# Optimization experiments

Hardware: AMD Instinct MI355X
Metric: run time of the kernel (lower is better)

## Reference

```python
import jax, jax.numpy as jnp
import numpy as np

N = 100000       # nodes
E = 1600000      # edges (before self-loops)
IN = 128         # input feature dim
HID = 16         # per-head hidden dim (layer 1)
HEADS = 8        # heads (layer 1)
OUT = 64         # output classes (layer 2, heads=1)
NEG_SLOPE = 0.2  # PyG GATConv default leaky relu slope


def setup_inputs() -> dict:
    key = jax.random.key(0)
    ks = jax.random.split(key, 10)
    s = 0.05
    return {
        "x": jax.random.normal(ks[0], (N, IN), jnp.float32),
        "edge_index": jax.random.randint(ks[1], (2, E), 0, N, dtype=jnp.int64),
        "W1": jax.random.normal(ks[2], (IN, HEADS * HID), jnp.float32) * s,
        "att_src1": jax.random.normal(ks[3], (HEADS, HID), jnp.float32) * s,
        "att_dst1": jax.random.normal(ks[4], (HEADS, HID), jnp.float32) * s,
        "bias1": jnp.zeros((HEADS * HID,), jnp.float32),
        "W2": jax.random.normal(ks[5], (HEADS * HID, OUT), jnp.float32) * s,
        "att_src2": jax.random.normal(ks[6], (1, OUT), jnp.float32) * s,
        "att_dst2": jax.random.normal(ks[7], (1, OUT), jnp.float32) * s,
        "bias2": jnp.zeros((OUT,), jnp.float32),
    }


def gat_conv(x, edge_index, W, att_src, att_dst, bias, heads, ch):
    """PyG GATConv: linear -> per-edge LeakyReLU score -> segment softmax over
    incoming edges -> scatter-sum aggregation. Self-loops added (PyG default)."""
    n = x.shape[0]
    loop = jnp.arange(n, dtype=edge_index.dtype)
    src = jnp.concatenate([edge_index[0], loop])  # [E2]
    dst = jnp.concatenate([edge_index[1], loop])  # [E2]

    h = (x @ W).reshape(n, heads, ch)                       # [N,H,C]
    a_src = jnp.einsum('nhc,hc->nh', h, att_src)            # [N,H]
    a_dst = jnp.einsum('nhc,hc->nh', h, att_dst)            # [N,H]

    e = a_src[src] + a_dst[dst]                             # [E2,H]
    e = jnp.where(e > 0, e, NEG_SLOPE * e)                  # leaky relu

    # numerically stable segment softmax over edges grouped by dst
    m = jax.ops.segment_max(e, dst, num_segments=n)         # [N,H]
    p = jnp.exp(e - m[dst])                                 # [E2,H]
    denom = jax.ops.segment_sum(p, dst, num_segments=n)     # [N,H]
    alpha = p / (denom[dst] + 1e-16)                        # [E2,H]

    out = jax.ops.segment_sum(h[src] * alpha[:, :, None], dst, num_segments=n)
    return out.reshape(n, heads * ch) + bias                # concat heads


def reference(x, edge_index, W1, att_src1, att_dst1, bias1, W2, att_src2, att_dst2, bias2):
    h = jax.nn.relu(gat_conv(x, edge_index, W1, att_src1, att_dst1, bias1, HEADS, HID))
    # dropout is identity in eval mode
    out = gat_conv(h, edge_index, W2, att_src2, att_dst2, bias2, 1, OUT)
    return jax.nn.log_softmax(out, axis=1)
```

## Files before the change

kernel.cpp:

```cpp
#include <hip/hip_runtime.h>
#include <hip/hip_bf16.h>

#define N_NODES 100000
#define N_EDGES 1600000
#define NEG_SLOPE 0.2f

#define BUCK_SHIFT 7
#define NBUCK ((N_NODES + 127) >> BUCK_SHIFT)
#define B1 256
#define CHUNK ((N_EDGES + B1 - 1) / B1)

#define SCAN_ITEMS 4
#define SCAN_BLK 256
#define SCAN_CHUNK (SCAN_BLK * SCAN_ITEMS)
#define NSCAN (NBUCK * B1)
#define SCAN_NB ((NSCAN + SCAN_CHUNK - 1) / SCAN_CHUNK)

typedef _Float16 f16;
typedef _Float16 f16x8 __attribute__((ext_vector_type(8)));
typedef _Float16 f16x2 __attribute__((ext_vector_type(2)));
typedef float f32x4 __attribute__((ext_vector_type(4)));
typedef float f32x2v __attribute__((ext_vector_type(2)));

__device__ __forceinline__ bool edges_are_i64(const void* p) {
    const unsigned long long* q = (const unsigned long long*)p;
    bool ok = true;
#pragma unroll
    for (int i = 0; i < 8; i++)
        if (q[i] >= (unsigned long long)N_NODES) ok = false;
    return ok;
}
__device__ __forceinline__ int edge_src(const void* ei, int j, bool i64) {
    return i64 ? (int)((const long long*)ei)[j] : ((const int*)ei)[j];
}
__device__ __forceinline__ int edge_dst(const void* ei, int j, bool i64) {
    return i64 ? (int)((const long long*)ei)[N_EDGES + j] : ((const int*)ei)[N_EDGES + j];
}

__device__ __forceinline__ void acc4(f32x4& a, float w, int u) {
    f32x2v p0 = __builtin_amdgcn_cvt_pk_f32_fp8(u, false);
    f32x2v p1 = __builtin_amdgcn_cvt_pk_f32_fp8(u, true);
    a[0] = fmaf(w, p0[0], a[0]);
    a[1] = fmaf(w, p0[1], a[1]);
    a[2] = fmaf(w, p1[0], a[2]);
    a[3] = fmaf(w, p1[1], a[3]);
}

__global__ __launch_bounds__(256) void bhist_k(const void* __restrict__ ei,
                                               int* __restrict__ bh) {
    __shared__ int hist[NBUCK];
    bool i64 = edges_are_i64(ei);
    int bl = blockIdx.x, t = threadIdx.x;
    for (int i = t; i < NBUCK; i += 256) hist[i] = 0;
    __syncthreads();
    int lo = bl * CHUNK, hi = min(lo + CHUNK, N_EDGES);
    for (int j = lo + t; j < hi; j += 256)
        atomicAdd(&hist[edge_dst(ei, j, i64) >> BUCK_SHIFT], 1);
    __syncthreads();
    for (int i = t; i < NBUCK; i += 256) bh[i * B1 + bl] = hist[i];
}

__global__ __launch_bounds__(SCAN_BLK) void scan1_k(const int* __restrict__ in,
                                                    int* __restrict__ outp,
                                                    int* __restrict__ bsum, int n) {
    __shared__ int lds[SCAN_BLK];
    int t = threadIdx.x, b = blockIdx.x;
    int base = b * SCAN_CHUNK + t * SCAN_ITEMS;
    int v[SCAN_ITEMS];
    int s = 0;
#pragma unroll
    for (int i = 0; i < SCAN_ITEMS; i++) {
        v[i] = (base + i < n) ? in[base + i] : 0;
        s += v[i];
    }
    lds[t] = s;
    __syncthreads();
    for (int o = 1; o < SCAN_BLK; o <<= 1) {
        int x = (t >= o) ? lds[t - o] : 0;
        __syncthreads();
        lds[t] += x;
        __syncthreads();
    }
    if (t == SCAN_BLK - 1) bsum[b] = lds[t];
    int run = lds[t] - s;
#pragma unroll
    for (int i = 0; i < SCAN_ITEMS; i++) {
        if (base + i < n) outp[base + i] = run;
        run += v[i];
    }
}

__global__ __launch_bounds__(256) void scan2_k(int* __restrict__ bsum, int nb) {
    __shared__ int lds[256];
    int t = threadIdx.x;
    int v = (t < nb) ? bsum[t] : 0;
    lds[t] = v;
    __syncthreads();
    for (int o = 1; o < 256; o <<= 1) {
        int x = (t >= o) ? lds[t - o] : 0;
        __syncthreads();
        lds[t] += x;
        __syncthreads();
    }
    if (t < nb) bsum[t] = lds[t] - v;
}

__global__ void scan3_k(int* __restrict__ outp, const int* __restrict__ bsum, int n) {
    int i = blockIdx.x * blockDim.x + threadIdx.x;
    if (i < n) outp[i] += bsum[i / SCAN_CHUNK];
}

__global__ __launch_bounds__(256) void bscatter_k(const void* __restrict__ ei,
                                                  const int* __restrict__ s,
                                                  int* __restrict__ be) {
    __shared__ int cur[NBUCK];
    bool i64 = edges_are_i64(ei);
    int bl = blockIdx.x, t = threadIdx.x;
    for (int i = t; i < NBUCK; i += 256) cur[i] = s[i * B1 + bl];
    __syncthreads();
    int lo = bl * CHUNK, hi = min(lo + CHUNK, N_EDGES);
    for (int j = lo + t; j < hi; j += 256) {
        int d = edge_dst(ei, j, i64);
        int sr = edge_src(ei, j, i64);
        int pos = atomicAdd(&cur[d >> BUCK_SHIFT], 1);
        be[pos] = (sr << BUCK_SHIFT) | (d & 127);
    }
}

__global__ __launch_bounds__(256) void bcsr_k(const int* __restrict__ s,
                                              const int* __restrict__ be,
                                              int* __restrict__ rp,
                                              int* __restrict__ csrc) {
    __shared__ int cnt[128];
    __shared__ int pre[128];
    int b = blockIdx.x, t = threadIdx.x;
    int beg = s[b * B1];
    int end = (b == NBUCK - 1) ? N_EDGES : s[(b + 1) * B1];
    if (t < 128) cnt[t] = 0;
    __syncthreads();
    for (int j = beg + t; j < end; j += 256)
        atomicAdd(&cnt[be[j] & 127], 1);
    __syncthreads();
    if (t < 128) pre[t] = cnt[t];
    __syncthreads();
    for (int o = 1; o < 128; o <<= 1) {
        int x = 0;
        if (t < 128 && t >= o) x = pre[t - o];
        __syncthreads();
        if (t < 128) pre[t] += x;
        __syncthreads();
    }
    if (t < 128) {
        int node = (b << BUCK_SHIFT) + t;
        int excl = pre[t] - cnt[t];
        if (node < N_NODES) rp[node] = beg + excl;
        cnt[t] = excl;
    }
    if (b == 0 && t == 0) rp[N_NODES] = N_EDGES;
    __syncthreads();
    for (int j = beg + t; j < end; j += 256) {
        int e = be[j];
        int pos = beg + atomicAdd(&cnt[e & 127], 1);
        csrc[pos] = e >> BUCK_SHIFT;
    }
}

template <int NCT>
__global__ void cvt_wfrag_k(const float* __restrict__ W, f16* __restrict__ wf) {
    int idx = blockIdx.x * blockDim.x + threadIdx.x;
    if (idx >= 4 * NCT * 512) return;
    int j = idx & 7;
    int lane = (idx >> 3) & 63;
    int ct = (idx >> 9) % NCT;
    int ks = (idx >> 9) / NCT;
    int k = ks * 32 + 8 * (lane >> 4) + j;
    int col = ct * 16 + (lane & 15);
    wf[idx] = (f16)W[k * (NCT * 16) + col];
}

template <int NCT, typename AT>
__global__ __launch_bounds__(256) void gemm_mfma(const AT* __restrict__ A,
                                                 const f16* __restrict__ wf,
                                                 f16* __restrict__ H, int n) {
    int lane = threadIdx.x & 63;
    int row0 = blockIdx.x * 64 + (threadIdx.x >> 6) * 16;
    int m = lane & 15, g = lane >> 4;
    f32x4 acc[NCT];
#pragma unroll
    for (int ct = 0; ct < NCT; ct++) acc[ct] = (f32x4){0.f, 0.f, 0.f, 0.f};

    int ar = row0 + m;
    if (ar >= n) ar = 0;
    const AT* arow = A + (size_t)ar * 128 + g * 8;
    const f16x8* bp = (const f16x8*)wf;
#pragma unroll
    for (int ks = 0; ks < 4; ks++) {
        f16x8 af;
        if constexpr (sizeof(AT) == 4) {
            const float4* p = (const float4*)(arow + ks * 32);
            float4 a = p[0], b = p[1];
            af[0] = (f16)a.x; af[1] = (f16)a.y; af[2] = (f16)a.z; af[3] = (f16)a.w;
            af[4] = (f16)b.x; af[5] = (f16)b.y; af[6] = (f16)b.z; af[7] = (f16)b.w;
        } else {
            af = *(const f16x8*)(arow + ks * 32);
        }
#pragma unroll
        for (int ct = 0; ct < NCT; ct++) {
            f16x8 bf = bp[(ks * NCT + ct) * 64 + lane];
            acc[ct] = __builtin_amdgcn_mfma_f32_16x16x32_f16(af, bf, acc[ct], 0, 0, 0);
        }
    }
#pragma unroll
    for (int ct = 0; ct < NCT; ct++)
#pragma unroll
        for (int r = 0; r < 4; r++) {
            int orow = row0 + g * 4 + r;
            if (orow < n) H[(size_t)orow * (NCT * 16) + ct * 16 + m] = (f16)acc[ct][r];
        }
}

template <int HEADS, int CH>
__global__ void att_scores(const f16* __restrict__ H, const float* __restrict__ att_s,
                           const float* __restrict__ att_d, float* __restrict__ a_s,
                           float* __restrict__ a_d, unsigned char* __restrict__ h8,
                           int n) {
    int idx = blockIdx.x * blockDim.x + threadIdx.x;
    if (idx >= n * HEADS) return;
    int node = idx / HEADS;
    int h = idx - node * HEADS;
    const f16x8* hp = (const f16x8*)(H + (size_t)node * (HEADS * CH) + h * CH);
    float vals[CH];
    float s = 0.f, d = 0.f;
#pragma unroll
    for (int c8 = 0; c8 < CH / 8; c8++) {
        f16x8 v = hp[c8];
#pragma unroll
        for (int j = 0; j < 8; j++) {
            float x = (float)v[j];
            vals[c8 * 8 + j] = x;
            s = fmaf(x, att_s[h * CH + c8 * 8 + j], s);
            d = fmaf(x, att_d[h * CH + c8 * 8 + j], d);
        }
    }
    a_s[idx] = s;
    a_d[idx] = d;

    int4* dst = (int4*)(h8 + (size_t)node * (HEADS * CH) + h * CH);
#pragma unroll
    for (int t = 0; t < CH / 16; t++) {
        int w[4];
#pragma unroll
        for (int q = 0; q < 4; q++) {
            int u = __builtin_amdgcn_cvt_pk_fp8_f32(vals[t * 16 + 4 * q],
                                                    vals[t * 16 + 4 * q + 1], 0, false);
            u = __builtin_amdgcn_cvt_pk_fp8_f32(vals[t * 16 + 4 * q + 2],
                                                vals[t * 16 + 4 * q + 3], u, true);
            w[q] = u;
        }
        dst[t] = make_int4(w[0], w[1], w[2], w[3]);
    }
}

__global__ __launch_bounds__(256) void aggr1_k(const int* __restrict__ rp,
                                               const int* __restrict__ csrc,
                                               const float* __restrict__ a_s,
                                               const float* __restrict__ a_d,
                                               const unsigned char* __restrict__ h8,
                                               const float* __restrict__ bias,
                                               f16* __restrict__ out) {
    int lane = threadIdx.x & 63;
    int d = blockIdx.x * 4 + (threadIdx.x >> 6);
    if (d >= N_NODES) return;
    int j = lane >> 4;
    int c = lane & 15;
    int head = c >> 1;

    float ed = a_d[d * 8 + head];
    f32x4 accA = {0.f, 0.f, 0.f, 0.f}, accB = {0.f, 0.f, 0.f, 0.f};
    float den = 0.f;

    if (j == 0) {
        float e0 = a_s[d * 8 + head] + ed;
        e0 = e0 > 0.f ? e0 : NEG_SLOPE * e0;
        float w0 = __expf(e0);
        den = w0;
        int2 u = *(const int2*)(h8 + (size_t)d * 128 + 8 * c);
        acc4(accA, w0, u.x); acc4(accB, w0, u.y);
    }

    int beg = rp[d], end = rp[d + 1];
    for (int cbeg = beg; cbeg < end; cbeg += 4) {
        int e = cbeg + j;
        int ee = e < end ? e : end - 1;
        int s = csrc[ee];
        float es = a_s[s * 8 + head] + ed;
        es = es > 0.f ? es : NEG_SLOPE * es;
        float w = (e < end) ? __expf(es) : 0.f;
        den += w;
        int2 u = *(const int2*)(h8 + (size_t)s * 128 + 8 * c);
        acc4(accA, w, u.x); acc4(accB, w, u.y);
    }

#pragma unroll
    for (int o = 16; o < 64; o <<= 1) {
        den += __shfl_xor(den, o, 64);
#pragma unroll
        for (int i = 0; i < 4; i++) {
            accA[i] += __shfl_xor(accA[i], o, 64);
            accB[i] += __shfl_xor(accB[i], o, 64);
        }
    }
    float inv = 1.f / (den + 1e-16f);

    f32x4 t = (j & 2) ? accB : accA;
    float vx = (j & 1) ? t[2] : t[0];
    float vy = (j & 1) ? t[3] : t[1];
    float2 b = ((const float2*)bias)[4 * c + j];
    f16x2 r;
    r[0] = (f16)fmaxf(fmaf(vx, inv, b.x), 0.f);
    r[1] = (f16)fmaxf(fmaf(vy, inv, b.y), 0.f);
    ((f16x2*)out)[(size_t)d * 64 + 4 * c + j] = r;
}

__global__ __launch_bounds__(256) void aggr2_k(const int* __restrict__ rp,
                                               const int* __restrict__ csrc,
                                               const float* __restrict__ a_s,
                                               const float* __restrict__ a_d,
                                               const unsigned char* __restrict__ h8,
                                               const float* __restrict__ bias,
                                               float* __restrict__ out) {
    int lane = threadIdx.x & 63;
    int d = blockIdx.x * 4 + (threadIdx.x >> 6);
    if (d >= N_NODES) return;
    int j = lane >> 3;
    int q = lane & 7;

    float ed = a_d[d];
    f32x4 accA = {0.f, 0.f, 0.f, 0.f}, accB = {0.f, 0.f, 0.f, 0.f};
    float den = 0.f;

    if (j == 0) {
        float e0 = a_s[d] + ed;
        e0 = e0 > 0.f ? e0 : NEG_SLOPE * e0;
        float w0 = __expf(e0);
        den = w0;
        int2 u = *(const int2*)(h8 + (size_t)d * 64 + 8 * q);
        acc4(accA, w0, u.x); acc4(accB, w0, u.y);
    }

    int beg = rp[d], end = rp[d + 1];
    for (int cbeg = beg; cbeg < end; cbeg += 8) {
        int e = cbeg + j;
        int ee = e < end ? e : end - 1;
        int s = csrc[ee];
        float es = a_s[s] + ed;
        es = es > 0.f ? es : NEG_SLOPE * es;
        float w = (e < end) ? __expf(es) : 0.f;
        den += w;
        int2 u = *(const int2*)(h8 + (size_t)s * 64 + 8 * q);
        acc4(accA, w, u.x); acc4(accB, w, u.y);
    }

#pragma unroll
    for (int o = 8; o < 64; o <<= 1) {
        den += __shfl_xor(den, o, 64);
#pragma unroll
        for (int i = 0; i < 4; i++) {
            accA[i] += __shfl_xor(accA[i], o, 64);
            accB[i] += __shfl_xor(accB[i], o, 64);
        }
    }
    float inv = 1.f / (den + 1e-16f);

    const float4* bp = (const float4*)bias;
    float4 b0 = bp[2 * q], b1 = bp[2 * q + 1];
    float z[8];
    z[0] = fmaf(accA[0], inv, b0.x); z[1] = fmaf(accA[1], inv, b0.y);
    z[2] = fmaf(accA[2], inv, b0.z); z[3] = fmaf(accA[3], inv, b0.w);
    z[4] = fmaf(accB[0], inv, b1.x); z[5] = fmaf(accB[1], inv, b1.y);
    z[6] = fmaf(accB[2], inv, b1.z); z[7] = fmaf(accB[3], inv, b1.w);

    float m = z[0];
#pragma unroll
    for (int i = 1; i < 8; i++) m = fmaxf(m, z[i]);
#pragma unroll
    for (int o = 1; o < 8; o <<= 1) m = fmaxf(m, __shfl_xor(m, o, 64));
    float p = 0.f;
#pragma unroll
    for (int i = 0; i < 8; i++) p += __expf(z[i] - m);
#pragma unroll
    for (int o = 1; o < 8; o <<= 1) p += __shfl_xor(p, o, 64);
    float lse = m + logf(p);

    if (j == 0) {
        float4 o0 = {z[0] - lse, z[1] - lse, z[2] - lse, z[3] - lse};
        float4 o1 = {z[4] - lse, z[5] - lse, z[6] - lse, z[7] - lse};
        float4* op = (float4*)(out + (size_t)d * 64 + 8 * q);
        op[0] = o0;
        op[1] = o1;
    }
}

extern "C" void kernel_launch(void* const* d_in, const int* in_sizes, int n_in,
                              void* d_out, int out_size, void* d_ws, size_t ws_size,
                              hipStream_t stream) {
    const float* x   = (const float*)d_in[0];
    const void*  ei  = d_in[1];
    const float* W1  = (const float*)d_in[2];
    const float* as1 = (const float*)d_in[3];
    const float* ad1 = (const float*)d_in[4];
    const float* b1  = (const float*)d_in[5];
    const float* W2  = (const float*)d_in[6];
    const float* as2 = (const float*)d_in[7];
    const float* ad2 = (const float*)d_in[8];
    const float* b2  = (const float*)d_in[9];
    float* out = (float*)d_out;

    f16*   h1   = (f16*)d_ws;
    f16*   out1 = h1 + (size_t)N_NODES * 128;
    unsigned char* h8 = (unsigned char*)(out1 + (size_t)N_NODES * 128);
    f16*   w1f  = (f16*)(h8 + (size_t)N_NODES * 128);
    f16*   w2f  = w1f + 16384;
    float* a_s  = (float*)(w2f + 8192);
    float* a_d  = a_s + (size_t)N_NODES * 8;
    int*   rp   = (int*)(a_d + (size_t)N_NODES * 8);
    int*   bh   = rp + (N_NODES + 64);
    int*   bsum = bh + NSCAN;
    int*   csrc = bsum + 256;
    int*   be   = csrc + N_EDGES;
    f16*   h2   = h1;

    bhist_k<<<B1, 256, 0, stream>>>(ei, bh);
    scan1_k<<<SCAN_NB, SCAN_BLK, 0, stream>>>(bh, bh, bsum, NSCAN);
    scan2_k<<<1, 256, 0, stream>>>(bsum, SCAN_NB);
    scan3_k<<<(NSCAN + 255) / 256, 256, 0, stream>>>(bh, bsum, NSCAN);
    bscatter_k<<<B1, 256, 0, stream>>>(ei, bh, be);
    bcsr_k<<<NBUCK, 256, 0, stream>>>(bh, be, rp, csrc);

    cvt_wfrag_k<8><<<(4 * 8 * 512 + 255) / 256, 256, 0, stream>>>(W1, w1f);
    cvt_wfrag_k<4><<<(4 * 4 * 512 + 255) / 256, 256, 0, stream>>>(W2, w2f);

    gemm_mfma<8, float><<<(N_NODES + 63) / 64, 256, 0, stream>>>(x, w1f, h1, N_NODES);
    att_scores<8, 16><<<(N_NODES * 8 + 255) / 256, 256, 0, stream>>>(h1, as1, ad1, a_s, a_d, h8, N_NODES);
    aggr1_k<<<(N_NODES + 3) / 4, 256, 0, stream>>>(rp, csrc, a_s, a_d, h8, b1, out1);

    gemm_mfma<4, f16><<<(N_NODES + 63) / 64, 256, 0, stream>>>(out1, w2f, h2, N_NODES);
    att_scores<1, 64><<<(N_NODES + 255) / 256, 256, 0, stream>>>(h2, as2, ad2, a_s, a_d, h8, N_NODES);
    aggr2_k<<<(N_NODES + 3) / 4, 256, 0, stream>>>(rp, csrc, a_s, a_d, h8, b2, out);
}
```

Before: 249.6 us.

## Precompute per-edge attention weights in edge-parallel kernels and restructure aggr1 lanes

Adds a CSR destination array and two edge-parallel kernels that compute exp(leaky_relu(a_s+a_d)) per edge ahead of time, f16 for layer 1 and fp32 for layer 2. The aggregation kernels then read these weights instead of recomputing them. aggr1 is restructured so each lane owns two output channels and broadcasts the per-edge weight and source index via swizzle and readlane, which removes the cross-lane reduction. The extra kernels add edge-sized memory traffic and two launches, and storing the layer-1 weights in f16 lowers their precision.

```diff
diff --git a/kernel.cpp b/kernel.cpp
--- a/kernel.cpp
+++ b/kernel.cpp
@@ -130,7 +130,8 @@
 __global__ __launch_bounds__(256) void bcsr_k(const int* __restrict__ s,
                                               const int* __restrict__ be,
                                               int* __restrict__ rp,
-                                              int* __restrict__ csrc) {
+                                              int* __restrict__ csrc,
+                                              int* __restrict__ cdst) {
     __shared__ int cnt[128];
     __shared__ int pre[128];
     int b = blockIdx.x, t = threadIdx.x;
@@ -162,7 +163,46 @@
         int e = be[j];
         int pos = beg + atomicAdd(&cnt[e & 127], 1);
         csrc[pos] = e >> BUCK_SHIFT;
-    }
+        cdst[pos] = (b << BUCK_SHIFT) | (e & 127);
+    }
+}
+
+__global__ __launch_bounds__(256) void ew1_k(const int* __restrict__ csrc,
+                                             const int* __restrict__ cdst,
+                                             const float* __restrict__ a_s,
+                                             const float* __restrict__ a_d,
+                                             f16* __restrict__ w1e) {
+    int e = blockIdx.x * 256 + threadIdx.x;
+    if (e >= N_EDGES) return;
+    int s = csrc[e], d = cdst[e];
+    const float4* as = (const float4*)(a_s + (size_t)s * 8);
+    const float4* ad = (const float4*)(a_d + (size_t)d * 8);
+    float4 s0 = as[0], s1 = as[1];
+    float4 d0 = ad[0], d1 = ad[1];
+    f16x8 w;
+    float t;
+    t = s0.x + d0.x; t = t > 0.f ? t : NEG_SLOPE * t; w[0] = (f16)__expf(t);
+    t = s0.y + d0.y; t = t > 0.f ? t : NEG_SLOPE * t; w[1] = (f16)__expf(t);
+    t = s0.z + d0.z; t = t > 0.f ? t : NEG_SLOPE * t; w[2] = (f16)__expf(t);
+    t = s0.w + d0.w; t = t > 0.f ? t : NEG_SLOPE * t; w[3] = (f16)__expf(t);
+    t = s1.x + d1.x; t = t > 0.f ? t : NEG_SLOPE * t; w[4] = (f16)__expf(t);
+    t = s1.y + d1.y; t = t > 0.f ? t : NEG_SLOPE * t; w[5] = (f16)__expf(t);
+    t = s1.z + d1.z; t = t > 0.f ? t : NEG_SLOPE * t; w[6] = (f16)__expf(t);
+    t = s1.w + d1.w; t = t > 0.f ? t : NEG_SLOPE * t; w[7] = (f16)__expf(t);
+    ((f16x8*)w1e)[e] = w;
+}
+
+__global__ __launch_bounds__(256) void ew2_k(const int* __restrict__ csrc,
+                                             const int* __restrict__ cdst,
+                                             const float* __restrict__ a_s,
+                                             const float* __restrict__ a_d,
+                                             float* __restrict__ w2e) {
+    int e = blockIdx.x * 256 + threadIdx.x;
+    if (e >= N_EDGES) return;
+    int s = csrc[e], d = cdst[e];
+    float t = a_s[s] + a_d[d];
+    t = t > 0.f ? t : NEG_SLOPE * t;
+    w2e[e] = __expf(t);
 }
 
 template <int NCT>
@@ -263,6 +303,7 @@
 
 __global__ __launch_bounds__(256) void aggr1_k(const int* __restrict__ rp,
                                                const int* __restrict__ csrc,
+                                               const f16* __restrict__ w1e,
                                                const float* __restrict__ a_s,
                                                const float* __restrict__ a_d,
                                                const unsigned char* __restrict__ h8,
@@ -271,59 +312,49 @@
     int lane = threadIdx.x & 63;
     int d = blockIdx.x * 4 + (threadIdx.x >> 6);
     if (d >= N_NODES) return;
-    int j = lane >> 4;
-    int c = lane & 15;
-    int head = c >> 1;
-
-    float ed = a_d[d * 8 + head];
-    f32x4 accA = {0.f, 0.f, 0.f, 0.f}, accB = {0.f, 0.f, 0.f, 0.f};
-    float den = 0.f;
-
-    if (j == 0) {
-        float e0 = a_s[d * 8 + head] + ed;
-        e0 = e0 > 0.f ? e0 : NEG_SLOPE * e0;
-        float w0 = __expf(e0);
-        den = w0;
-        int2 u = *(const int2*)(h8 + (size_t)d * 128 + 8 * c);
-        acc4(accA, w0, u.x); acc4(accB, w0, u.y);
-    }
+    int head = lane >> 3;
+    int eidx = lane & 7;
+
+    float e0 = a_s[d * 8 + head] + a_d[d * 8 + head];
+    e0 = e0 > 0.f ? e0 : NEG_SLOPE * e0;
+    float w0 = __expf(e0);
+    unsigned short u0 = *(const unsigned short*)(h8 + (size_t)d * 128 + 2 * lane);
+    f32x2v v0 = __builtin_amdgcn_cvt_pk_f32_fp8((int)u0, false);
+    float den = w0, nx = w0 * v0[0], ny = w0 * v0[1];
 
     int beg = rp[d], end = rp[d + 1];
-    for (int cbeg = beg; cbeg < end; cbeg += 4) {
-        int e = cbeg + j;
+    for (int cbeg = beg; cbeg < end; cbeg += 8) {
+        int e = cbeg + eidx;
         int ee = e < end ? e : end - 1;
         int s = csrc[ee];
-        float es = a_s[s * 8 + head] + ed;
-        es = es > 0.f ? es : NEG_SLOPE * es;
-        float w = (e < end) ? __expf(es) : 0.f;
-        den += w;
-        int2 u = *(const int2*)(h8 + (size_t)s * 128 + 8 * c);
-        acc4(accA, w, u.x); acc4(accB, w, u.y);
-    }
-
-#pragma unroll
-    for (int o = 16; o < 64; o <<= 1) {
-        den += __shfl_xor(den, o, 64);
-#pragma unroll
-        for (int i = 0; i < 4; i++) {
-            accA[i] += __shfl_xor(accA[i], o, 64);
-            accB[i] += __shfl_xor(accB[i], o, 64);
-        }
+        float w = (float)w1e[(size_t)ee * 8 + head];
+        if (e >= end) w = 0.f;
+#define A1_STEP(K)                                                                       \
+        {                                                                                \
+            float we = __int_as_float(__builtin_amdgcn_ds_swizzle(                        \
+                __float_as_int(w), ((K) << 5) | 0x18));                                  \
+            int se = __builtin_amdgcn_readlane(s, (K));                                  \
+            unsigned short uu = *(const unsigned short*)(h8 + (size_t)se * 128 + 2 * lane); \
+            f32x2v v = __builtin_amdgcn_cvt_pk_f32_fp8((int)uu, false);                  \
+            den += we;                                                                   \
+            nx = fmaf(we, v[0], nx);                                                     \
+            ny = fmaf(we, v[1], ny);                                                     \
+        }
+        A1_STEP(0) A1_STEP(1) A1_STEP(2) A1_STEP(3)
+        A1_STEP(4) A1_STEP(5) A1_STEP(6) A1_STEP(7)
+#undef A1_STEP
     }
     float inv = 1.f / (den + 1e-16f);
-
-    f32x4 t = (j & 2) ? accB : accA;
-    float vx = (j & 1) ? t[2] : t[0];
-    float vy = (j & 1) ? t[3] : t[1];
-    float2 b = ((const float2*)bias)[4 * c + j];
+    float2 b = ((const float2*)bias)[lane];
     f16x2 r;
-    r[0] = (f16)fmaxf(fmaf(vx, inv, b.x), 0.f);
-    r[1] = (f16)fmaxf(fmaf(vy, inv, b.y), 0.f);
-    ((f16x2*)out)[(size_t)d * 64 + 4 * c + j] = r;
+    r[0] = (f16)fmaxf(fmaf(nx, inv, b.x), 0.f);
+    r[1] = (f16)fmaxf(fmaf(ny, inv, b.y), 0.f);
+    ((f16x2*)out)[(size_t)d * 64 + lane] = r;
 }
 
 __global__ __launch_bounds__(256) void aggr2_k(const int* __restrict__ rp,
                                                const int* __restrict__ csrc,
+                                               const float* __restrict__ w2e,
                                                const float* __restrict__ a_s,
                                                const float* __restrict__ a_d,
                                                const unsigned char* __restrict__ h8,
@@ -335,12 +366,11 @@
     int j = lane >> 3;
     int q = lane & 7;
 
-    float ed = a_d[d];
     f32x4 accA = {0.f, 0.f, 0.f, 0.f}, accB = {0.f, 0.f, 0.f, 0.f};
     float den = 0.f;
 
     if (j == 0) {
-        float e0 = a_s[d] + ed;
+        float e0 = a_s[d] + a_d[d];
         e0 = e0 > 0.f ? e0 : NEG_SLOPE * e0;
         float w0 = __expf(e0);
         den = w0;
@@ -353,9 +383,8 @@
         int e = cbeg + j;
         int ee = e < end ? e : end - 1;
         int s = csrc[ee];
-        float es = a_s[s] + ed;
-        es = es > 0.f ? es : NEG_SLOPE * es;
-        float w = (e < end) ? __expf(es) : 0.f;
+        float w = w2e[ee];
+        if (e >= end) w = 0.f;
         den += w;
         int2 u = *(const int2*)(h8 + (size_t)s * 64 + 8 * q);
         acc4(accA, w, u.x); acc4(accB, w, u.y);
@@ -427,7 +456,10 @@
     int*   bh   = rp + (N_NODES + 64);
     int*   bsum = bh + NSCAN;
     int*   csrc = bsum + 256;
-    int*   be   = csrc + N_EDGES;
+    int*   cdst = csrc + N_EDGES;
+    float* w2e  = (float*)(cdst + N_EDGES);
+    f16*   w1e  = (f16*)(w2e + N_EDGES);
+    int*   be   = (int*)w1e;
     f16*   h2   = h1;
 
     bhist_k<<<B1, 256, 0, stream>>>(ei, bh);
@@ -435,16 +467,18 @@
     scan2_k<<<1, 256, 0, stream>>>(bsum, SCAN_NB);
     scan3_k<<<(NSCAN + 255) / 256, 256, 0, stream>>>(bh, bsum, NSCAN);
     bscatter_k<<<B1, 256, 0, stream>>>(ei, bh, be);
-    bcsr_k<<<NBUCK, 256, 0, stream>>>(bh, be, rp, csrc);
+    bcsr_k<<<NBUCK, 256, 0, stream>>>(bh, be, rp, csrc, cdst);
 
     cvt_wfrag_k<8><<<(4 * 8 * 512 + 255) / 256, 256, 0, stream>>>(W1, w1f);
     cvt_wfrag_k<4><<<(4 * 4 * 512 + 255) / 256, 256, 0, stream>>>(W2, w2f);
 
     gemm_mfma<8, float><<<(N_NODES + 63) / 64, 256, 0, stream>>>(x, w1f, h1, N_NODES);
     att_scores<8, 16><<<(N_NODES * 8 + 255) / 256, 256, 0, stream>>>(h1, as1, ad1, a_s, a_d, h8, N_NODES);
-    aggr1_k<<<(N_NODES + 3) / 4, 256, 0, stream>>>(rp, csrc, a_s, a_d, h8, b1, out1);
+    ew1_k<<<(N_EDGES + 255) / 256, 256, 0, stream>>>(csrc, cdst, a_s, a_d, w1e);
+    aggr1_k<<<(N_NODES + 3) / 4, 256, 0, stream>>>(rp, csrc, w1e, a_s, a_d, h8, b1, out1);
 
     gemm_mfma<4, f16><<<(N_NODES + 63) / 64, 256, 0, stream>>>(out1, w2f, h2, N_NODES);
     att_scores<1, 64><<<(N_NODES + 255) / 256, 256, 0, stream>>>(h2, as2, ad2, a_s, a_d, h8, N_NODES);
-    aggr2_k<<<(N_NODES + 3) / 4, 256, 0, stream>>>(rp, csrc, a_s, a_d, h8, b2, out);
-}
+    ew2_k<<<(N_EDGES + 255) / 256, 256, 0, stream>>>(csrc, cdst, a_s, a_d, w2e);
+    aggr2_k<<<(N_NODES + 3) / 4, 256, 0, stream>>>(rp, csrc, w2e, a_s, a_d, h8, b2, out);
+}
```

Result: faster. 238.0 us (-4.7%).

## Fold scan fixup into consumers and restructure layer-1 aggregation per head

Applied to the files above, without the earlier changes.

Removes the scan3 kernel by adding block sums on the fly where bucket offsets are read in bscatter and bcsr. Rewrites aggr1 so each lane owns two output channels, with each group of 8 lanes handling one head and 8 edges per step. Source indices are broadcast with readlane and edge weights with ds_swizzle, which removes the final cross-lane reduction. Both aggregation kernels also prefetch the next batch of csrc indices to hide index-load latency. The cost is narrower 2-byte gathers per lane in aggr1, more loads issued per iteration, and more wasted lanes on nodes with few edges.

```diff
diff --git a/kernel.cpp b/kernel.cpp
--- a/kernel.cpp
+++ b/kernel.cpp
@@ -105,18 +105,17 @@
     if (t < nb) bsum[t] = lds[t] - v;
 }
 
-__global__ void scan3_k(int* __restrict__ outp, const int* __restrict__ bsum, int n) {
-    int i = blockIdx.x * blockDim.x + threadIdx.x;
-    if (i < n) outp[i] += bsum[i / SCAN_CHUNK];
-}
-
 __global__ __launch_bounds__(256) void bscatter_k(const void* __restrict__ ei,
-                                                  const int* __restrict__ s,
+                                                  const int* __restrict__ bh,
+                                                  const int* __restrict__ bsum,
                                                   int* __restrict__ be) {
     __shared__ int cur[NBUCK];
     bool i64 = edges_are_i64(ei);
     int bl = blockIdx.x, t = threadIdx.x;
-    for (int i = t; i < NBUCK; i += 256) cur[i] = s[i * B1 + bl];
+    for (int i = t; i < NBUCK; i += 256) {
+        int idx = i * B1 + bl;
+        cur[i] = bh[idx] + bsum[idx / SCAN_CHUNK];
+    }
     __syncthreads();
     int lo = bl * CHUNK, hi = min(lo + CHUNK, N_EDGES);
     for (int j = lo + t; j < hi; j += 256) {
@@ -127,15 +126,21 @@
     }
 }
 
-__global__ __launch_bounds__(256) void bcsr_k(const int* __restrict__ s,
+__global__ __launch_bounds__(256) void bcsr_k(const int* __restrict__ bh,
+                                              const int* __restrict__ bsum,
                                               const int* __restrict__ be,
                                               int* __restrict__ rp,
                                               int* __restrict__ csrc) {
     __shared__ int cnt[128];
     __shared__ int pre[128];
     int b = blockIdx.x, t = threadIdx.x;
-    int beg = s[b * B1];
-    int end = (b == NBUCK - 1) ? N_EDGES : s[(b + 1) * B1];
+    int bi = b * B1;
+    int beg = bh[bi] + bsum[bi / SCAN_CHUNK];
+    int end = N_EDGES;
+    if (b != NBUCK - 1) {
+        int bj = (b + 1) * B1;
+        end = bh[bj] + bsum[bj / SCAN_CHUNK];
+    }
     if (t < 128) cnt[t] = 0;
     __syncthreads();
     for (int j = beg + t; j < end; j += 256)
@@ -271,55 +276,62 @@
     int lane = threadIdx.x & 63;
     int d = blockIdx.x * 4 + (threadIdx.x >> 6);
     if (d >= N_NODES) return;
-    int j = lane >> 4;
-    int c = lane & 15;
-    int head = c >> 1;
+    int head = lane >> 3;
+    int eidx = lane & 7;
 
     float ed = a_d[d * 8 + head];
-    f32x4 accA = {0.f, 0.f, 0.f, 0.f}, accB = {0.f, 0.f, 0.f, 0.f};
-    float den = 0.f;
-
-    if (j == 0) {
-        float e0 = a_s[d * 8 + head] + ed;
-        e0 = e0 > 0.f ? e0 : NEG_SLOPE * e0;
-        float w0 = __expf(e0);
-        den = w0;
-        int2 u = *(const int2*)(h8 + (size_t)d * 128 + 8 * c);
-        acc4(accA, w0, u.x); acc4(accB, w0, u.y);
-    }
+
+    float e0 = a_s[d * 8 + head] + ed;
+    e0 = e0 > 0.f ? e0 : NEG_SLOPE * e0;
+    float w0 = __expf(e0);
+    unsigned short u0 = *(const unsigned short*)(h8 + (size_t)d * 128 + 2 * lane);
+    f32x2v v0 = __builtin_amdgcn_cvt_pk_f32_fp8((int)u0, false);
+    float den = w0, nx = w0 * v0[0], ny = w0 * v0[1];
 
     int beg = rp[d], end = rp[d + 1];
-    for (int cbeg = beg; cbeg < end; cbeg += 4) {
-        int e = cbeg + j;
-        int ee = e < end ? e : end - 1;
-        int s = csrc[ee];
-        float es = a_s[s * 8 + head] + ed;
+    int s_cur = 0;
+    if (beg < end) {
+        int e = beg + eidx;
+        s_cur = csrc[e < end ? e : end - 1];
+    }
+    for (int cbeg = beg; cbeg < end; cbeg += 8) {
+        int s = s_cur;
+        if (cbeg + 8 < end) {
+            int e = cbeg + 8 + eidx;
+            s_cur = csrc[e < end ? e : end - 1];
+        }
+        unsigned short uu0, uu1, uu2, uu3, uu4, uu5, uu6, uu7;
+#define A1_LOAD(K)                                                                        \
+        {                                                                                 \
+            int se = __builtin_amdgcn_readlane(s, K);                                     \
+            uu##K = *(const unsigned short*)(h8 + (size_t)se * 128 + 2 * lane);           \
+        }
+        A1_LOAD(0) A1_LOAD(1) A1_LOAD(2) A1_LOAD(3)
+        A1_LOAD(4) A1_LOAD(5) A1_LOAD(6) A1_LOAD(7)
+#undef A1_LOAD
+        float as = a_s[s * 8 + head];
+        float es = as + ed;
         es = es > 0.f ? es : NEG_SLOPE * es;
-        float w = (e < end) ? __expf(es) : 0.f;
-        den += w;
-        int2 u = *(const int2*)(h8 + (size_t)s * 128 + 8 * c);
-        acc4(accA, w, u.x); acc4(accB, w, u.y);
-    }
-
-#pragma unroll
-    for (int o = 16; o < 64; o <<= 1) {
-        den += __shfl_xor(den, o, 64);
-#pragma unroll
-        for (int i = 0; i < 4; i++) {
-            accA[i] += __shfl_xor(accA[i], o, 64);
-            accB[i] += __shfl_xor(accB[i], o, 64);
-        }
+        float w = (cbeg + eidx < end) ? __expf(es) : 0.f;
+#define A1_USE(K)                                                                         \
+        {                                                                                 \
+            float we = __int_as_float(__builtin_amdgcn_ds_swizzle(                         \
+                __float_as_int(w), ((K) << 5) | 0x18));                                   \
+            f32x2v v = __builtin_amdgcn_cvt_pk_f32_fp8((int)uu##K, false);                \
+            den += we;                                                                    \
+            nx = fmaf(we, v[0], nx);                                                      \
+            ny = fmaf(we, v[1], ny);                                                      \
+        }
+        A1_USE(0) A1_USE(1) A1_USE(2) A1_USE(3)
+        A1_USE(4) A1_USE(5) A1_USE(6) A1_USE(7)
+#undef A1_USE
     }
     float inv = 1.f / (den + 1e-16f);
-
-    f32x4 t = (j & 2) ? accB : accA;
-    float vx = (j & 1) ? t[2] : t[0];
-    float vy = (j & 1) ? t[3] : t[1];
-    float2 b = ((const float2*)bias)[4 * c + j];
+    float2 b = ((const float2*)bias)[lane];
     f16x2 r;
-    r[0] = (f16)fmaxf(fmaf(vx, inv, b.x), 0.f);
-    r[1] = (f16)fmaxf(fmaf(vy, inv, b.y), 0.f);
-    ((f16x2*)out)[(size_t)d * 64 + 4 * c + j] = r;
+    r[0] = (f16)fmaxf(fmaf(nx, inv, b.x), 0.f);
+    r[1] = (f16)fmaxf(fmaf(ny, inv, b.y), 0.f);
+    ((f16x2*)out)[(size_t)d * 64 + lane] = r;
 }
 
 __global__ __launch_bounds__(256) void aggr2_k(const int* __restrict__ rp,
@@ -349,15 +361,23 @@
     }
 
     int beg = rp[d], end = rp[d + 1];
+    int s_cur = 0;
+    if (beg < end) {
+        int e = beg + j;
+        s_cur = csrc[e < end ? e : end - 1];
+    }
     for (int cbeg = beg; cbeg < end; cbeg += 8) {
-        int e = cbeg + j;
-        int ee = e < end ? e : end - 1;
-        int s = csrc[ee];
-        float es = a_s[s] + ed;
+        int s = s_cur;
+        if (cbeg + 8 < end) {
+            int e = cbeg + 8 + j;
+            s_cur = csrc[e < end ? e : end - 1];
+        }
+        int2 u = *(const int2*)(h8 + (size_t)s * 64 + 8 * q);
+        float as = a_s[s];
+        float es = as + ed;
         es = es > 0.f ? es : NEG_SLOPE * es;
-        float w = (e < end) ? __expf(es) : 0.f;
+        float w = (cbeg + j < end) ? __expf(es) : 0.f;
         den += w;
-        int2 u = *(const int2*)(h8 + (size_t)s * 64 + 8 * q);
         acc4(accA, w, u.x); acc4(accB, w, u.y);
     }
 
@@ -433,9 +453,8 @@
     bhist_k<<<B1, 256, 0, stream>>>(ei, bh);
     scan1_k<<<SCAN_NB, SCAN_BLK, 0, stream>>>(bh, bh, bsum, NSCAN);
     scan2_k<<<1, 256, 0, stream>>>(bsum, SCAN_NB);
-    scan3_k<<<(NSCAN + 255) / 256, 256, 0, stream>>>(bh, bsum, NSCAN);
-    bscatter_k<<<B1, 256, 0, stream>>>(ei, bh, be);
-    bcsr_k<<<NBUCK, 256, 0, stream>>>(bh, be, rp, csrc);
+    bscatter_k<<<B1, 256, 0, stream>>>(ei, bh, bsum, be);
+    bcsr_k<<<NBUCK, 256, 0, stream>>>(bh, bsum, be, rp, csrc);
 
     cvt_wfrag_k<8><<<(4 * 8 * 512 + 255) / 256, 256, 0, stream>>>(W1, w1f);
     cvt_wfrag_k<4><<<(4 * 4 * 512 + 255) / 256, 256, 0, stream>>>(W2, w2f);
```

Result: faster. 204.4 us (-18.1%).
